# Optimization experiments

Hardware: AMD Instinct MI355X
Metric: run time of the kernel (lower is better)

Reference implementation:

```python
import jax, jax.numpy as jnp
import numpy as np

B, N, HD = 2, 2048, 2048
NH, KVH = 16, 4
D = HD // NH          # 128
R = NH // KVH         # 4 (kv_ratio)
KVD = KVH * D         # 512


def setup_inputs() -> dict:
    key = jax.random.key(0)
    ks = jax.random.split(key, 6)
    s = 0.02
    return {
        "tokens": jax.random.normal(ks[0], (B, N, HD), jnp.float32),
        "norm_w": jnp.ones((HD,), jnp.float32),
        "Wq": jax.random.normal(ks[1], (HD, HD), jnp.float32) * s,
        "bq": jnp.zeros((HD,), jnp.float32),
        "Wk": jax.random.normal(ks[2], (KVD, HD), jnp.float32) * s,
        "bk": jnp.zeros((KVD,), jnp.float32),
        "Wv": jax.random.normal(ks[3], (KVD, HD), jnp.float32) * s,
        "bv": jnp.zeros((KVD,), jnp.float32),
        "Wo": jax.random.normal(ks[4], (HD, HD), jnp.float32) * s,
        "bo": jnp.zeros((HD,), jnp.float32),
    }


def reference(tokens, norm_w, Wq, bq, Wk, bk, Wv, bv, Wo, bo):
    # RMSNorm (torch default eps=None -> finfo eps), learnable weight
    eps = jnp.finfo(tokens.dtype).eps
    x = tokens * jax.lax.rsqrt(jnp.mean(tokens * tokens, axis=-1, keepdims=True) + eps) * norm_w

    # projections -> [B, heads, N, D]
    q = (x @ Wq.T + bq).reshape(B, N, NH, D).transpose(0, 2, 1, 3)
    k = (x @ Wk.T + bk).reshape(B, N, KVH, D).transpose(0, 2, 1, 3)
    v = (x @ Wv.T + bv).reshape(B, N, KVH, D).transpose(0, 2, 1, 3)

    # GQA via tiling the kv block (matches torch.cat of copies: head h uses kv head h % KVH)
    k = jnp.tile(k, (1, R, 1, 1))
    v = jnp.tile(v, (1, R, 1, 1))

    # Faithful (inverted) mask: True where j <= i, and True positions are masked out.
    mask = jnp.arange(N)[None, :] <= jnp.arange(N)[:, None]  # [N, N]

    # No 1/sqrt(D) scaling in the original
    scores = jnp.einsum('bhid,bhjd->bhij', q, k)
    scores = jnp.where(mask[None, None, :, :], jnp.float32(-1e9), scores)
    attn = jax.nn.softmax(scores, axis=-1)

    a = jnp.einsum('bhij,bhjd->bhid', attn, v)       # [B, NH, N, D]
    a = a.transpose(0, 2, 1, 3).reshape(B, N, HD)    # [B, N, HD]
    return a @ Wo.T + bo
```

## Files before the change

### kernel.cpp

```cpp
#include <hip/hip_runtime.h>

#define BB   2
#define NN   2048
#define HDIM 2048
#define NHD  16
#define KVHD 4
#define DD   128
#define KVW  1024
#define MTOK (BB*NN)

typedef _Float16 h8 __attribute__((ext_vector_type(8)));
typedef _Float16 h4 __attribute__((ext_vector_type(4)));
typedef float    f4 __attribute__((ext_vector_type(4)));
typedef float    fx16 __attribute__((ext_vector_type(16)));
typedef short    b8 __attribute__((ext_vector_type(8)));
typedef unsigned int u4v __attribute__((ext_vector_type(4)));

static __device__ __forceinline__ f4 mfma16(h8 a, h8 b, f4 c) {
    return __builtin_amdgcn_mfma_f32_16x16x32_f16(a, b, c, 0, 0, 0);
}
static __device__ __forceinline__ fx16 mfma32b(b8 a, b8 b, fx16 c) {
    return __builtin_amdgcn_mfma_f32_32x32x16_bf16(a, b, c, 0, 0, 0);
}

static __device__ __forceinline__ unsigned short f2bf(float f) {
    unsigned int u = __float_as_uint(f);
    u += 0x7FFF + ((u >> 16) & 1);
    return (unsigned short)(u >> 16);
}

static __device__ __forceinline__ void gload_lds16(const void* g, void* l) {
    __builtin_amdgcn_global_load_lds(
        (const __attribute__((address_space(1))) void*)g,
        (__attribute__((address_space(3))) void*)l, 16, 0, 0);
}

__global__ __launch_bounds__(256) void rmsnorm_k(const float* __restrict__ t,
                                                 const float* __restrict__ wn,
                                                 _Float16* __restrict__ xh) {
    const int row = blockIdx.x, tid = threadIdx.x;
    const float* rp = t + (size_t)row * HDIM;
    float4 v[2];
    float ss = 0.f;
    #pragma unroll
    for (int p = 0; p < 2; ++p) {
        float4 x = *(const float4*)(rp + (p * 256 + tid) * 4);
        v[p] = x;
        ss += x.x * x.x + x.y * x.y + x.z * x.z + x.w * x.w;
    }
    #pragma unroll
    for (int off = 32; off; off >>= 1) ss += __shfl_xor(ss, off, 64);
    __shared__ float sred[4];
    if ((tid & 63) == 0) sred[tid >> 6] = ss;
    __syncthreads();
    float rs = rsqrtf((sred[0] + sred[1] + sred[2] + sred[3]) * (1.0f / HDIM)
                      + 1.1920928955078125e-07f);
    _Float16* op = xh + (size_t)row * HDIM;
    #pragma unroll
    for (int p = 0; p < 2; ++p) {
        int base = (p * 256 + tid) * 4;
        float4 w = *(const float4*)(wn + base);
        h4 o;
        o[0] = (_Float16)(v[p].x * rs * w.x);
        o[1] = (_Float16)(v[p].y * rs * w.y);
        o[2] = (_Float16)(v[p].z * rs * w.z);
        o[3] = (_Float16)(v[p].w * rs * w.w);
        *(h4*)(op + base) = o;
    }
}

__global__ __launch_bounds__(256) void cvt_k(const float* __restrict__ src,
                                             _Float16* __restrict__ dst, int n) {
    int i = (blockIdx.x * 256 + threadIdx.x) * 4;
    if (i < n) {
        float4 v = *(const float4*)(src + i);
        h4 o; o[0] = (_Float16)v.x; o[1] = (_Float16)v.y;
        o[2] = (_Float16)v.z; o[3] = (_Float16)v.w;
        *(h4*)(dst + i) = o;
    }
}

__global__ void biascat_k(const float* __restrict__ bk, const float* __restrict__ bv,
                          float* __restrict__ bkv, float* __restrict__ vsum) {
    int i = blockIdx.x * 256 + threadIdx.x;
    bkv[i] = (i < 512) ? bk[i] : bv[i - 512];
    vsum[i] = 0.f;
}

__global__ __launch_bounds__(256) void vtrans_k(const _Float16* __restrict__ kv,
                                                unsigned short* __restrict__ vt) {
    const int tid = threadIdx.x;
    const int tok = blockIdx.x * 64 + (tid & 63);
    const int kvh = blockIdx.y;
    const int d0 = (tid >> 6) * 32;
    const int b = tok >> 11, n = tok & (NN - 1);
    const _Float16* src = kv + (size_t)tok * KVW + 512 + kvh * DD + d0;
    unsigned short* dstb = vt + ((size_t)(b * KVHD + kvh) * DD) * NN + n;
    #pragma unroll
    for (int u = 0; u < 4; ++u) {
        h8 v = *(const h8*)(src + u * 8);
        #pragma unroll
        for (int e = 0; e < 8; ++e)
            dstb[(size_t)(d0 + u * 8 + e) * NN] = f2bf((float)v[e]);
    }
}

template <int OUTF32>
__global__ __launch_bounds__(256, 2) void gemm_bt(const _Float16* __restrict__ A,
                                                  const _Float16* __restrict__ Bw,
                                                  const float* __restrict__ bias,
                                                  void* __restrict__ Cout,
                                                  int Ndim, int K) {
    __shared__ _Float16 sA[128 * 64];
    __shared__ _Float16 sB[128 * 64];
    const int tid = threadIdx.x;
    const int lane = tid & 63, w = tid >> 6;
    const int ln = lane & 15, quad = lane >> 4;
    const int wm = w >> 1, wn = w & 1;
    const int m0 = blockIdx.y * 128, n0 = blockIdx.x * 128;

    f4 acc[4][4] = {};
    for (int k0 = 0; k0 < K; k0 += 64) {
        #pragma unroll
        for (int it = 0; it < 4; ++it) {
            int chunk = it * 256 + tid;
            int row = chunk >> 3, p = chunk & 7;
            int c = p ^ (row & 7);
            gload_lds16(A + (size_t)(m0 + row) * K + k0 + c * 8, sA + chunk * 8);
            gload_lds16(Bw + (size_t)(n0 + row) * K + k0 + c * 8, sB + chunk * 8);
        }
        __syncthreads();
        #pragma unroll
        for (int kk = 0; kk < 2; ++kk) {
            h8 af[4], bf[4];
            #pragma unroll
            for (int mt = 0; mt < 4; ++mt)
                af[mt] = *(const h8*)&sA[(wm * 64 + mt * 16 + ln) * 64 +
                                         (((kk * 4 + quad) ^ (ln & 7)) << 3)];
            #pragma unroll
            for (int nt = 0; nt < 4; ++nt)
                bf[nt] = *(const h8*)&sB[(wn * 64 + nt * 16 + ln) * 64 +
                                         (((kk * 4 + quad) ^ (ln & 7)) << 3)];
            #pragma unroll
            for (int mt = 0; mt < 4; ++mt)
                #pragma unroll
                for (int nt = 0; nt < 4; ++nt)
                    acc[mt][nt] = mfma16(af[mt], bf[nt], acc[mt][nt]);
        }
        __syncthreads();
    }
    #pragma unroll
    for (int mt = 0; mt < 4; ++mt) {
        int rowb = m0 + wm * 64 + mt * 16 + quad * 4;
        #pragma unroll
        for (int nt = 0; nt < 4; ++nt) {
            int col = n0 + wn * 64 + nt * 16 + ln;
            float bv = bias[col];
            #pragma unroll
            for (int r = 0; r < 4; ++r) {
                float v = acc[mt][nt][r] + bv;
                if (OUTF32)
                    ((float*)Cout)[(size_t)(rowb + r) * Ndim + col] = v;
                else
                    ((_Float16*)Cout)[(size_t)(rowb + r) * Ndim + col] = (_Float16)v;
            }
        }
    }
}

__global__ __launch_bounds__(256, 2) void attn_k(const _Float16* __restrict__ qh,
                                                 const _Float16* __restrict__ kvp,
                                                 const unsigned short* __restrict__ vt,
                                                 _Float16* __restrict__ ah) {
    __shared__ _Float16 s_k[2][64 * 128];
    __shared__ unsigned short s_v[2][128 * 64];
    const int tid = threadIdx.x;
    const int lane = tid & 63, w = tid >> 6;
    const int ln = lane & 15, quad = lane >> 4;
    const int l5 = lane & 31, hi = lane >> 5;
    const int sel = quad & 1;
    const int h = blockIdx.y, b = blockIdx.z;
    const int it0 = b ? (15 - (int)blockIdx.x) : (int)blockIdx.x;
    const int i0 = it0 * 128;
    const int kvh = h & 3;

    h8 qf[2][4];
    #pragma unroll
    for (int t = 0; t < 2; ++t) {
        const _Float16* qrow =
            qh + ((size_t)(b * NN + i0 + w * 32 + t * 16 + ln)) * HDIM + h * DD;
        #pragma unroll
        for (int kc = 0; kc < 4; ++kc)
            qf[t][kc] = *(const h8*)(qrow + kc * 32 + quad * 8);
    }

    b8 ones;
    #pragma unroll
    for (int e = 0; e < 8; ++e) ones[e] = (short)0x3F80;

    fx16 O[4] = {};
    fx16 OS = {};

    auto stage = [&](int jt, int bufi) {
        const int j0s = jt * 64;
        #pragma unroll
        for (int itr = 0; itr < 4; ++itr) {
            int chunk = itr * 256 + tid;
            int jj = chunk >> 4, p = chunk & 15;
            int c = p ^ (jj & 15);
            gload_lds16(kvp + ((size_t)(b * NN + j0s + jj)) * KVW + kvh * DD + c * 8,
                        &s_k[bufi][chunk * 8]);
        }
        #pragma unroll
        for (int itr = 0; itr < 4; ++itr) {
            int chunk = itr * 256 + tid;
            int d = chunk >> 3, p = chunk & 7;
            int c = p ^ (d & 7);
            gload_lds16(vt + ((size_t)(b * KVHD + kvh) * DD + d) * NN + j0s + c * 8,
                        &s_v[bufi][chunk * 8]);
        }
    };

    const int jt0 = it0 * 2;
    stage(jt0, 0);
    for (int jt = jt0; jt < 32; ++jt) {
        const int j0 = jt * 64;
        const int cur = (jt - jt0) & 1;
        __syncthreads();
        if (jt + 1 < 32) stage(jt + 1, cur ^ 1);

        f4 sc[2][4] = {};
        #pragma unroll
        for (int nt = 0; nt < 4; ++nt)
            #pragma unroll
            for (int kc = 0; kc < 4; ++kc) {
                h8 kf = *(const h8*)&s_k[cur][(nt * 16 + ln) * 128 +
                                              (((kc * 4 + quad) ^ ln) << 3)];
                sc[0][nt] = mfma16(kf, qf[0][kc], sc[0][nt]);
                sc[1][nt] = mfma16(kf, qf[1][kc], sc[1][nt]);
            }

        const bool need_mask = (jt < jt0 + 2);
        unsigned int u0[4][2], u1[4][2];
        #pragma unroll
        for (int nt = 0; nt < 4; ++nt)
            #pragma unroll
            for (int rr = 0; rr < 2; ++rr) {
                float a0 = sc[0][nt][2 * rr], a1 = sc[0][nt][2 * rr + 1];
                float c0 = sc[1][nt][2 * rr], c1 = sc[1][nt][2 * rr + 1];
                if (need_mask) {
                    int jg = j0 + nt * 16 + quad * 4 + 2 * rr;
                    int ig0 = i0 + w * 32 + ln;
                    int ig1 = ig0 + 16;
                    if (jg <= ig0) a0 = -1e9f;
                    if (jg + 1 <= ig0) a1 = -1e9f;
                    if (jg <= ig1) c0 = -1e9f;
                    if (jg + 1 <= ig1) c1 = -1e9f;
                }
                u0[nt][rr] = (unsigned int)f2bf(__expf(a0)) |
                             ((unsigned int)f2bf(__expf(a1)) << 16);
                u1[nt][rr] = (unsigned int)f2bf(__expf(c0)) |
                             ((unsigned int)f2bf(__expf(c1)) << 16);
            }

        b8 paf[4];
        #pragma unroll
        for (int nt = 0; nt < 4; ++nt) {
            unsigned int own0 = sel ? u1[nt][0] : u0[nt][0];
            unsigned int own1 = sel ? u1[nt][1] : u0[nt][1];
            unsigned int oth0 = sel ? u0[nt][0] : u1[nt][0];
            unsigned int oth1 = sel ? u0[nt][1] : u1[nt][1];
            unsigned int r0 = __shfl_xor(oth0, 16, 64);
            unsigned int r1 = __shfl_xor(oth1, 16, 64);
            u4v pw;
            pw[0] = sel ? r0 : own0;
            pw[1] = sel ? r1 : own1;
            pw[2] = sel ? own0 : r0;
            pw[3] = sel ? own1 : r1;
            paf[nt] = __builtin_bit_cast(b8, pw);
        }

        #pragma unroll
        for (int nt = 0; nt < 4; ++nt) {
            #pragma unroll
            for (int dblk = 0; dblk < 4; ++dblk) {
                b8 bv = *(const b8*)&s_v[cur][(dblk * 32 + l5) * 64 +
                                              (((nt * 2 + hi) ^ (l5 & 7)) << 3)];
                O[dblk] = mfma32b(paf[nt], bv, O[dblk]);
            }
            OS = mfma32b(paf[nt], ones, OS);
        }
    }

    float inv_l[16];
    #pragma unroll
    for (int rg = 0; rg < 16; ++rg) inv_l[rg] = 1.0f / OS[rg];
    #pragma unroll
    for (int nt4 = 0; nt4 < 4; ++nt4)
        #pragma unroll
        for (int rg = 0; rg < 16; ++rg) {
            int q = (rg & 3) + 8 * (rg >> 2) + 4 * hi;
            ah[((size_t)(b * NN + i0 + w * 32 + q)) * HDIM + h * DD + nt4 * 32 + l5] =
                (_Float16)(O[nt4][rg] * inv_l[rg]);
        }
}

__global__ __launch_bounds__(256) void vsum_k(const _Float16* __restrict__ kvp,
                                              float* __restrict__ vsum) {
    __shared__ float red[16][128];
    const int seg = blockIdx.x, kvh = blockIdx.y, b = blockIdx.z;
    const int tid = threadIdx.x;
    const int jj = tid >> 4, dc = (tid & 15) * 8;
    float acc[8] = {};
    #pragma unroll 4
    for (int j = seg * 256 + jj; j < seg * 256 + 256; j += 16) {
        h8 v = *(const h8*)(kvp + ((size_t)(b * NN + j)) * KVW + 512 + kvh * DD + dc);
        #pragma unroll
        for (int e = 0; e < 8; ++e) acc[e] += (float)v[e];
    }
    #pragma unroll
    for (int e = 0; e < 8; ++e) red[jj][dc + e] = acc[e];
    __syncthreads();
    if (tid < 128) {
        float s = 0.f;
        #pragma unroll
        for (int t = 0; t < 16; ++t) s += red[t][tid];
        atomicAdd(&vsum[(b * KVHD + kvh) * DD + tid], s);
    }
}

__global__ void fixup_write_k(const float* __restrict__ vsum,
                              _Float16* __restrict__ ah) {
    int b = blockIdx.x >> 2, kvh = blockIdx.x & 3, d = threadIdx.x;
    float mean = vsum[(b * KVHD + kvh) * DD + d] * (1.0f / NN);
    #pragma unroll
    for (int r = 0; r < 4; ++r) {
        int h = r * 4 + kvh;
        ah[((size_t)(b * NN + NN - 1)) * HDIM + h * DD + d] = (_Float16)mean;
    }
}

extern "C" void kernel_launch(void* const* d_in, const int* in_sizes, int n_in,
                              void* d_out, int out_size, void* d_ws, size_t ws_size,
                              hipStream_t stream) {
    const float* tokens = (const float*)d_in[0];
    const float* norm_w = (const float*)d_in[1];
    const float* Wq = (const float*)d_in[2];
    const float* bq = (const float*)d_in[3];
    const float* Wk = (const float*)d_in[4];
    const float* bk = (const float*)d_in[5];
    const float* Wv = (const float*)d_in[6];
    const float* bv = (const float*)d_in[7];
    const float* Wo = (const float*)d_in[8];
    const float* bo = (const float*)d_in[9];
    float* out = (float*)d_out;

    char* ws = (char*)d_ws;
    _Float16* x_h   = (_Float16*)(ws);
    _Float16* wq_h  = (_Float16*)(ws + 16777216);
    _Float16* wkv_h = (_Float16*)(ws + 25165824);
    _Float16* wo_h  = (_Float16*)(ws + 29360128);
    float*    bkv   = (float*)   (ws + 37748736);
    _Float16* q_h   = (_Float16*)(ws + 37752832);
    _Float16* kv_h  = (_Float16*)(ws + 54530048);
    _Float16* a_h   = (_Float16*)(ws + 62918656);
    unsigned short* vt_h = (unsigned short*)(ws + 79695872);
    float*    vsum  = (float*)   (ws + 83890176);

    rmsnorm_k<<<MTOK, 256, 0, stream>>>(tokens, norm_w, x_h);
    cvt_k<<<4096, 256, 0, stream>>>(Wq, wq_h, HDIM * HDIM);
    cvt_k<<<1024, 256, 0, stream>>>(Wk, wkv_h, 512 * HDIM);
    cvt_k<<<1024, 256, 0, stream>>>(Wv, wkv_h + 512 * HDIM, 512 * HDIM);
    cvt_k<<<4096, 256, 0, stream>>>(Wo, wo_h, HDIM * HDIM);
    biascat_k<<<4, 256, 0, stream>>>(bk, bv, bkv, vsum);

    gemm_bt<0><<<dim3(HDIM / 128, MTOK / 128), 256, 0, stream>>>(
        x_h, wq_h, bq, (void*)q_h, HDIM, HDIM);
    gemm_bt<0><<<dim3(KVW / 128, MTOK / 128), 256, 0, stream>>>(
        x_h, wkv_h, bkv, (void*)kv_h, KVW, HDIM);

    vtrans_k<<<dim3(MTOK / 64, KVHD), 256, 0, stream>>>(kv_h, vt_h);

    attn_k<<<dim3(16, NHD, BB), 256, 0, stream>>>(q_h, kv_h, vt_h, a_h);
    vsum_k<<<dim3(8, KVHD, BB), 256, 0, stream>>>(kv_h, vsum);
    fixup_write_k<<<BB * KVHD, 128, 0, stream>>>(vsum, a_h);

    gemm_bt<1><<<dim3(HDIM / 128, MTOK / 128), 256, 0, stream>>>(
        a_h, wo_h, bo, (void*)out, HDIM, HDIM);
}
```

Baseline: 325.7 us.

## Split long causal attention row-tiles across two blocks and fuse QKV GEMM

Row tiles 0-6 have the most key tiles under the inverted causal mask. Each of them is now split into two key ranges handled by separate blocks, which write unnormalized fp32 partial outputs and row sums to a workspace; a new combine kernel adds the pairs and normalizes. Each remaining block handles one tile, so the grid goes from 16 to 23 blocks per head and the per-block work is more even, aiming to cut the long-block tail. Separately, the Q and KV projections become one GEMM launch over a concatenated bias, with the output routed to two destinations. The cost is an extra kernel launch and fp32 partial-output traffic through a workspace that reuses the dead activation and weight region.

```diff
diff --git a/kernel.cpp b/kernel.cpp
--- a/kernel.cpp
+++ b/kernel.cpp
@@ -8,6 +8,7 @@
 #define DD   128
 #define KVW  1024
 #define MTOK (BB*NN)
+#define NSPLIT 7
 
 typedef _Float16 h8 __attribute__((ext_vector_type(8)));
 typedef _Float16 h4 __attribute__((ext_vector_type(4)));
@@ -80,11 +81,12 @@
     }
 }
 
-__global__ void biascat_k(const float* __restrict__ bk, const float* __restrict__ bv,
-                          float* __restrict__ bkv, float* __restrict__ vsum) {
+__global__ void biascat_k(const float* __restrict__ bq, const float* __restrict__ bk,
+                          const float* __restrict__ bv,
+                          float* __restrict__ bqkv, float* __restrict__ vsum) {
     int i = blockIdx.x * 256 + threadIdx.x;
-    bkv[i] = (i < 512) ? bk[i] : bv[i - 512];
-    vsum[i] = 0.f;
+    bqkv[i] = (i < 2048) ? bq[i] : (i < 2560) ? bk[i - 2048] : bv[i - 2560];
+    if (i < 1024) vsum[i] = 0.f;
 }
 
 __global__ __launch_bounds__(256) void vtrans_k(const _Float16* __restrict__ kv,
@@ -105,11 +107,12 @@
     }
 }
 
-template <int OUTF32>
+template <int MODE>
 __global__ __launch_bounds__(256, 2) void gemm_bt(const _Float16* __restrict__ A,
                                                   const _Float16* __restrict__ Bw,
                                                   const float* __restrict__ bias,
                                                   void* __restrict__ Cout,
+                                                  void* __restrict__ Cout2,
                                                   int Ndim, int K) {
     __shared__ _Float16 sA[128 * 64];
     __shared__ _Float16 sB[128 * 64];
@@ -159,10 +162,16 @@
             #pragma unroll
             for (int r = 0; r < 4; ++r) {
                 float v = acc[mt][nt][r] + bv;
-                if (OUTF32)
+                if (MODE == 1)
                     ((float*)Cout)[(size_t)(rowb + r) * Ndim + col] = v;
-                else
+                else if (MODE == 0)
                     ((_Float16*)Cout)[(size_t)(rowb + r) * Ndim + col] = (_Float16)v;
+                else {
+                    if (n0 < 2048)
+                        ((_Float16*)Cout)[(size_t)(rowb + r) * HDIM + col] = (_Float16)v;
+                    else
+                        ((_Float16*)Cout2)[(size_t)(rowb + r) * KVW + (col - 2048)] = (_Float16)v;
+                }
             }
         }
     }
@@ -171,7 +180,9 @@
 __global__ __launch_bounds__(256, 2) void attn_k(const _Float16* __restrict__ qh,
                                                  const _Float16* __restrict__ kvp,
                                                  const unsigned short* __restrict__ vt,
-                                                 _Float16* __restrict__ ah) {
+                                                 _Float16* __restrict__ ah,
+                                                 float* __restrict__ O_ws,
+                                                 float* __restrict__ l_ws) {
     __shared__ _Float16 s_k[2][64 * 128];
     __shared__ unsigned short s_v[2][128 * 64];
     const int tid = threadIdx.x;
@@ -180,9 +191,17 @@
     const int l5 = lane & 31, hi = lane >> 5;
     const int sel = quad & 1;
     const int h = blockIdx.y, b = blockIdx.z;
-    const int it0 = b ? (15 - (int)blockIdx.x) : (int)blockIdx.x;
-    const int i0 = it0 * 128;
     const int kvh = h & 3;
+
+    const int k = blockIdx.x;
+    int x, jlo, jhi, p = 0;
+    bool is_split = false;
+    if (k == 0)       { x = 7; jlo = 14; jhi = 32; }
+    else if (k < 15)  { x = (k - 1) >> 1; p = (k - 1) & 1;
+                        int len = 16 - x;
+                        jlo = 2 * x + p * len; jhi = jlo + len; is_split = true; }
+    else              { x = 8 + (k - 15); jlo = 2 * x; jhi = 32; }
+    const int i0 = x * 128;
 
     h8 qf[2][4];
     #pragma unroll
@@ -206,28 +225,27 @@
         #pragma unroll
         for (int itr = 0; itr < 4; ++itr) {
             int chunk = itr * 256 + tid;
-            int jj = chunk >> 4, p = chunk & 15;
-            int c = p ^ (jj & 15);
+            int jj = chunk >> 4, pp = chunk & 15;
+            int c = pp ^ (jj & 15);
             gload_lds16(kvp + ((size_t)(b * NN + j0s + jj)) * KVW + kvh * DD + c * 8,
                         &s_k[bufi][chunk * 8]);
         }
         #pragma unroll
         for (int itr = 0; itr < 4; ++itr) {
             int chunk = itr * 256 + tid;
-            int d = chunk >> 3, p = chunk & 7;
-            int c = p ^ (d & 7);
+            int d = chunk >> 3, pp = chunk & 7;
+            int c = pp ^ (d & 7);
             gload_lds16(vt + ((size_t)(b * KVHD + kvh) * DD + d) * NN + j0s + c * 8,
                         &s_v[bufi][chunk * 8]);
         }
     };
 
-    const int jt0 = it0 * 2;
-    stage(jt0, 0);
-    for (int jt = jt0; jt < 32; ++jt) {
+    stage(jlo, 0);
+    for (int jt = jlo; jt < jhi; ++jt) {
         const int j0 = jt * 64;
-        const int cur = (jt - jt0) & 1;
+        const int cur = (jt - jlo) & 1;
         __syncthreads();
-        if (jt + 1 < 32) stage(jt + 1, cur ^ 1);
+        if (jt + 1 < jhi) stage(jt + 1, cur ^ 1);
 
         f4 sc[2][4] = {};
         #pragma unroll
@@ -240,7 +258,7 @@
                 sc[1][nt] = mfma16(kf, qf[1][kc], sc[1][nt]);
             }
 
-        const bool need_mask = (jt < jt0 + 2);
+        const bool need_mask = (jt < 2 * x + 2);
         unsigned int u0[4][2], u1[4][2];
         #pragma unroll
         for (int nt = 0; nt < 4; ++nt)
@@ -292,17 +310,55 @@
         }
     }
 
-    float inv_l[16];
-    #pragma unroll
-    for (int rg = 0; rg < 16; ++rg) inv_l[rg] = 1.0f / OS[rg];
-    #pragma unroll
-    for (int nt4 = 0; nt4 < 4; ++nt4)
-        #pragma unroll
-        for (int rg = 0; rg < 16; ++rg) {
-            int q = (rg & 3) + 8 * (rg >> 2) + 4 * hi;
-            ah[((size_t)(b * NN + i0 + w * 32 + q)) * HDIM + h * DD + nt4 * 32 + l5] =
-                (_Float16)(O[nt4][rg] * inv_l[rg]);
-        }
+    if (is_split) {
+        size_t po = (((size_t)(b * NHD + h) * NSPLIT + x) * 2 + p);
+        float* Op = O_ws + po * 16384;
+        float* Lp = l_ws + po * 128;
+        #pragma unroll
+        for (int nt4 = 0; nt4 < 4; ++nt4)
+            #pragma unroll
+            for (int rg = 0; rg < 16; ++rg) {
+                int q = (rg & 3) + 8 * (rg >> 2) + 4 * hi;
+                Op[(w * 32 + q) * 128 + nt4 * 32 + l5] = O[nt4][rg];
+            }
+        if (l5 == 0) {
+            #pragma unroll
+            for (int rg = 0; rg < 16; ++rg) {
+                int q = (rg & 3) + 8 * (rg >> 2) + 4 * hi;
+                Lp[w * 32 + q] = OS[rg];
+            }
+        }
+    } else {
+        float inv_l[16];
+        #pragma unroll
+        for (int rg = 0; rg < 16; ++rg) inv_l[rg] = 1.0f / OS[rg];
+        #pragma unroll
+        for (int nt4 = 0; nt4 < 4; ++nt4)
+            #pragma unroll
+            for (int rg = 0; rg < 16; ++rg) {
+                int q = (rg & 3) + 8 * (rg >> 2) + 4 * hi;
+                ah[((size_t)(b * NN + i0 + w * 32 + q)) * HDIM + h * DD + nt4 * 32 + l5] =
+                    (_Float16)(O[nt4][rg] * inv_l[rg]);
+            }
+    }
+}
+
+__global__ __launch_bounds__(256) void combine_k(const float* __restrict__ O_ws,
+                                                 const float* __restrict__ l_ws,
+                                                 _Float16* __restrict__ ah) {
+    const int x = blockIdx.x, h = blockIdx.y, b = blockIdx.z;
+    const int tid = threadIdx.x;
+    const int d = tid & 127;
+    size_t po = (((size_t)(b * NHD + h) * NSPLIT + x) * 2);
+    const float* O0 = O_ws + po * 16384;
+    const float* O1 = O0 + 16384;
+    const float* L0 = l_ws + po * 128;
+    const float* L1 = L0 + 128;
+    for (int ql = tid >> 7; ql < 128; ql += 2) {
+        float l = L0[ql] + L1[ql];
+        float o = O0[ql * 128 + d] + O1[ql * 128 + d];
+        ah[((size_t)(b * NN + x * 128 + ql)) * HDIM + h * DD + d] = (_Float16)(o / l);
+    }
 }
 
 __global__ __launch_bounds__(256) void vsum_k(const _Float16* __restrict__ kvp,
@@ -360,31 +416,32 @@
     _Float16* wq_h  = (_Float16*)(ws + 16777216);
     _Float16* wkv_h = (_Float16*)(ws + 25165824);
     _Float16* wo_h  = (_Float16*)(ws + 29360128);
-    float*    bkv   = (float*)   (ws + 37748736);
     _Float16* q_h   = (_Float16*)(ws + 37752832);
     _Float16* kv_h  = (_Float16*)(ws + 54530048);
     _Float16* a_h   = (_Float16*)(ws + 62918656);
     unsigned short* vt_h = (unsigned short*)(ws + 79695872);
     float*    vsum  = (float*)   (ws + 83890176);
+    float*    l_ws  = (float*)   (ws + 83894272);
+    float*    bqkv  = (float*)   (ws + 84123648);
+    float*    O_ws  = (float*)(ws);
 
     rmsnorm_k<<<MTOK, 256, 0, stream>>>(tokens, norm_w, x_h);
     cvt_k<<<4096, 256, 0, stream>>>(Wq, wq_h, HDIM * HDIM);
     cvt_k<<<1024, 256, 0, stream>>>(Wk, wkv_h, 512 * HDIM);
     cvt_k<<<1024, 256, 0, stream>>>(Wv, wkv_h + 512 * HDIM, 512 * HDIM);
     cvt_k<<<4096, 256, 0, stream>>>(Wo, wo_h, HDIM * HDIM);
-    biascat_k<<<4, 256, 0, stream>>>(bk, bv, bkv, vsum);
-
-    gemm_bt<0><<<dim3(HDIM / 128, MTOK / 128), 256, 0, stream>>>(
-        x_h, wq_h, bq, (void*)q_h, HDIM, HDIM);
-    gemm_bt<0><<<dim3(KVW / 128, MTOK / 128), 256, 0, stream>>>(
-        x_h, wkv_h, bkv, (void*)kv_h, KVW, HDIM);
+    biascat_k<<<12, 256, 0, stream>>>(bq, bk, bv, bqkv, vsum);
+
+    gemm_bt<2><<<dim3(3072 / 128, MTOK / 128), 256, 0, stream>>>(
+        x_h, wq_h, bqkv, (void*)q_h, (void*)kv_h, 3072, HDIM);
 
     vtrans_k<<<dim3(MTOK / 64, KVHD), 256, 0, stream>>>(kv_h, vt_h);
 
-    attn_k<<<dim3(16, NHD, BB), 256, 0, stream>>>(q_h, kv_h, vt_h, a_h);
+    attn_k<<<dim3(23, NHD, BB), 256, 0, stream>>>(q_h, kv_h, vt_h, a_h, O_ws, l_ws);
+    combine_k<<<dim3(NSPLIT, NHD, BB), 256, 0, stream>>>(O_ws, l_ws, a_h);
     vsum_k<<<dim3(8, KVHD, BB), 256, 0, stream>>>(kv_h, vsum);
     fixup_write_k<<<BB * KVHD, 128, 0, stream>>>(vsum, a_h);
 
     gemm_bt<1><<<dim3(HDIM / 128, MTOK / 128), 256, 0, stream>>>(
-        a_h, wo_h, bo, (void*)out, HDIM, HDIM);
-}
+        a_h, wo_h, bo, (void*)out, nullptr, HDIM, HDIM);
+}
```

New measurement: 318.1 us. 1.02x faster.
